# Optimization experiments

Measured on AMD Instinct MI355X. Metric: run time of the kernel, lower is better.

The kernel has to match this reference:

```python
import jax, jax.numpy as jnp
import numpy as np
from jax import lax

B, C_KEY, H, W = 2, 512, 48, 48
HW = H * W
TOPK = 4


def _conv(x, w, b, pad):
    # x: NCHW, w: OIHW (torch Conv2d layout)
    y = lax.conv_general_dilated(x, w, (1, 1), [(pad, pad), (pad, pad)],
                                 dimension_numbers=('NCHW', 'OIHW', 'NCHW'))
    return y + b[None, :, None, None]


def _deconv(x, w, b, stride, pad):
    # torch ConvTranspose2d weight layout (in_c, out_c, kh, kw).
    # Equivalent dilated conv: flip kernel spatially, swap in/out,
    # lhs_dilation=stride, padding=k-1-p each side.
    k = w.shape[2]
    kern = jnp.transpose(jnp.flip(w, (2, 3)), (1, 0, 2, 3))  # OIHW
    y = lax.conv_general_dilated(x, kern, (1, 1),
                                 [(k - 1 - pad, k - 1 - pad)] * 2,
                                 lhs_dilation=(stride, stride),
                                 dimension_numbers=('NCHW', 'OIHW', 'NCHW'))
    return y + b[None, :, None, None]


def setup_inputs() -> dict:
    key = jax.random.key(0)
    ks = jax.random.split(key, 32)

    def nrm(i, shape, scale=1.0):
        return jax.random.normal(ks[i], shape, jnp.float32) * scale

    def unit_key(i):
        k_ = jax.random.normal(ks[i], (B, C_KEY, H, W), jnp.float32)
        return k_ / jnp.linalg.norm(k_, axis=1, keepdims=True)

    inp = {
        'feats_s16': nrm(0, (B, 1024, H, W)),
        'feats_s8': nrm(1, (B, 512, 2 * H, 2 * W)),
        'feats_s4': nrm(2, (B, 256, 4 * H, 4 * W)),
        'key': unit_key(3),
        'init_key': unit_key(4),
        'prev_key': unit_key(5),
        'init_seg_16': jax.random.uniform(ks[6], (B, 2, H, W), jnp.float32),
        'prev_seg_16': jax.random.uniform(ks[7], (B, 2, H, W), jnp.float32),
        'mask_feats': nrm(8, (B, 256, H, W), 0.1),
        # Decoder parameters (torch layouts)
        'w_conv1': nrm(9, (256, 1024, 1, 1), 0.03), 'b_conv1': jnp.zeros((256,), jnp.float32),
        'w_blend1': nrm(10, (256, 516, 3, 3), 0.02), 'b_blend1': jnp.zeros((256,), jnp.float32),
        'w_deconv1': nrm(11, (256, 2, 4, 4), 0.02), 'b_deconv1': jnp.zeros((2,), jnp.float32),
        'w_conv2': nrm(12, (256, 512, 1, 1), 0.04), 'b_conv2': jnp.zeros((256,), jnp.float32),
        'w_blend2': nrm(13, (256, 258, 3, 3), 0.02), 'b_blend2': jnp.zeros((256,), jnp.float32),
        'w_deconv2': nrm(14, (256, 2, 4, 4), 0.02), 'b_deconv2': jnp.zeros((2,), jnp.float32),
        'w_conv3': nrm(15, (256, 256, 1, 1), 0.06), 'b_conv3': jnp.zeros((256,), jnp.float32),
        'w_blend3': nrm(16, (256, 258, 3, 3), 0.02), 'b_blend3': jnp.zeros((256,), jnp.float32),
        'w_deconv3': nrm(17, (256, 2, 6, 6), 0.02), 'b_deconv3': jnp.zeros((2,), jnp.float32),
    }
    return inp


def _forward(feats_s16, feats_s8, feats_s4, key, init_key, prev_key,
             init_seg_16, prev_seg_16, mask_feats,
             w_conv1, b_conv1, w_blend1, b_blend1, w_deconv1, b_deconv1,
             w_conv2, b_conv2, w_blend2, b_blend2, w_deconv2, b_deconv2,
             w_conv3, b_conv3, w_blend3, b_blend3, w_deconv3, b_deconv3):
    relu = jax.nn.relu
    Bn, _, Hh, Ww = key.shape
    HWn = Hh * Ww

    kf = key.reshape(Bn, -1, HWn)
    # cosine similarities mapped to [0,1]; p = ref pixel, q = query pixel
    global_sim = (jnp.einsum('bcp,bcq->bpq', init_key.reshape(Bn, -1, HWn), kf) + 1.0) * 0.5
    local_sim = (jnp.einsum('bcp,bcq->bpq', prev_key.reshape(Bn, -1, HWn), kf) + 1.0) * 0.5

    def global_score(seg_ch):  # seg_ch: (B,H,W)
        s = global_sim * seg_ch.reshape(Bn, HWn, 1)
        return jnp.max(s, axis=1)  # (B,HW)

    def local_score(seg_ch):
        s = local_sim * seg_ch.reshape(Bn, HWn, 1)  # (B,HW,HW)
        cut = lax.top_k(s, TOPK)[0][..., -1:]       # kth-largest along key dim
        mn = jnp.min(s, axis=2, keepdims=True)
        s = jnp.where(s < cut, mn, s)               # threshold masking
        return jnp.max(s, axis=1)                   # (B,HW)

    matching_score = jnp.stack([
        global_score(init_seg_16[:, 0]),
        global_score(init_seg_16[:, 1]),
        local_score(prev_seg_16[:, 0]),
        local_score(prev_seg_16[:, 1]),
    ], axis=1).reshape(Bn, 4, Hh, Ww)

    # Decoder
    x = jnp.concatenate([relu(_conv(feats_s16, w_conv1, b_conv1, 0)),
                         matching_score, mask_feats], axis=1)
    s8 = _deconv(relu(_conv(x, w_blend1, b_blend1, 1)), w_deconv1, b_deconv1, 2, 1)
    x = jnp.concatenate([relu(_conv(feats_s8, w_conv2, b_conv2, 0)), s8], axis=1)
    s4 = _deconv(relu(_conv(x, w_blend2, b_blend2, 1)), w_deconv2, b_deconv2, 2, 1)
    x = jnp.concatenate([relu(_conv(feats_s4, w_conv3, b_conv3, 0)), s4], axis=1)
    final_score = _deconv(relu(_conv(x, w_blend3, b_blend3, 1)), w_deconv3, b_deconv3, 4, 1)
    return final_score


def reference(feats_s16, feats_s8, feats_s4, key, init_key, prev_key,
              init_seg_16, prev_seg_16, mask_feats,
              w_conv1, b_conv1, w_blend1, b_blend1, w_deconv1, b_deconv1,
              w_conv2, b_conv2, w_blend2, b_blend2, w_deconv2, b_deconv2,
              w_conv3, b_conv3, w_blend3, b_blend3, w_deconv3, b_deconv3):
    return _forward(feats_s16, feats_s8, feats_s4, key, init_key, prev_key,
                    init_seg_16, prev_seg_16, mask_feats,
                    w_conv1, b_conv1, w_blend1, b_blend1, w_deconv1, b_deconv1,
                    w_conv2, b_conv2, w_blend2, b_blend2, w_deconv2, b_deconv2,
                    w_conv3, b_conv3, w_blend3, b_blend3, w_deconv3, b_deconv3)
```

## Files before the change

### kernel.cpp

```cpp
#include <hip/hip_runtime.h>
#include <cstdio>

typedef unsigned short u16;
typedef __attribute__((ext_vector_type(4))) float f32x4;
typedef __attribute__((ext_vector_type(8))) short s16x8;
typedef __attribute__((ext_vector_type(4))) unsigned short u16x4;

#define DEV static __device__ __forceinline__

DEV float bf2f(u16 u) { union { unsigned int i; float f; } v; v.i = ((unsigned int)u) << 16; return v.f; }
DEV u16 f2bf(float f) {
  unsigned int x = __float_as_uint(f);
  unsigned int r = (x + 0x7fffu + ((x >> 16) & 1u)) >> 16;
  return (u16)r;
}

typedef const __attribute__((address_space(1))) unsigned int* gptr_t;
typedef __attribute__((address_space(3))) unsigned int* lptr_t;
DEV void gl16(const u16* g, u16* l) {
  __builtin_amdgcn_global_load_lds((gptr_t)g, (lptr_t)l, 16, 0, 0);
}

__global__ __launch_bounds__(256) void trans_key(const float* __restrict__ X,
    u16* __restrict__ Y)
{
  __shared__ u16 t[64][72];
  const int tid = threadIdx.x;
  const int n0 = blockIdx.x * 64, k0 = blockIdx.y * 64, b = blockIdx.z;
  const float* Xb = X + (size_t)b * 512 * 2304;
  const int nl = tid & 63, kr = tid >> 6;
#pragma unroll
  for (int kk = 0; kk < 16; ++kk) {
    int kl = kr + kk * 4;
    t[kl][nl] = f2bf(Xb[(size_t)(k0 + kl) * 2304 + n0 + nl]);
  }
  __syncthreads();
  const int nr = tid >> 2, kb = (tid & 3) * 16;
  u16* yp = Y + (size_t)b * 2304 * 512 + (size_t)(n0 + nr) * 512 + k0 + kb;
#pragma unroll
  for (int i = 0; i < 4; ++i) {
    u16x4 v;
#pragma unroll
    for (int e = 0; e < 4; ++e) v[e] = t[kb + i * 4 + e][nr];
    *(u16x4*)&yp[i * 4] = v;
  }
}

template<int MB>
__global__ __launch_bounds__(256) void sim_gemm_gl(const u16* __restrict__ AT,
    const u16* __restrict__ BT, float* __restrict__ out)
{
  constexpr int SUB = MB / 16, SPW = SUB / 4;
  __shared__ alignas(16) u16 Al[2][SUB][64][8];
  __shared__ alignas(16) u16 Bl[2][4][64][8];
  const int tid = threadIdx.x;
  const int n0 = blockIdx.x * 64, m0 = blockIdx.y * MB, b = blockIdx.z;
  const int lane = tid & 63, wv = tid >> 6;
  const int fr = lane & 15, kq = lane >> 4;
  const u16* Ab = AT + (size_t)b * 2304 * 512;
  const u16* Bb = BT + (size_t)b * 2304 * 512;
  f32x4 acc[SPW][4];
#pragma unroll
  for (int p = 0; p < SPW; ++p)
#pragma unroll
    for (int j = 0; j < 4; ++j) acc[p][j] = (f32x4){0, 0, 0, 0};
  auto ISSUE = [&](int buf, int s) {
    const int k0 = s * 32 + kq * 8;
    gl16(&Bb[(size_t)(n0 + wv * 16 + fr) * 512 + k0], &Bl[buf][wv][0][0]);
#pragma unroll
    for (int p = 0; p < SPW; ++p)
      gl16(&Ab[(size_t)(m0 + (wv * SPW + p) * 16 + fr) * 512 + k0],
           &Al[buf][wv * SPW + p][0][0]);
  };
  ISSUE(0, 0);
  __syncthreads();
  const int NS = 512 / 32;
  for (int s = 0; s < NS; ++s) {
    const int cur = s & 1;
    if (s + 1 < NS) ISSUE(cur ^ 1, s + 1);
    s16x8 bf[4];
#pragma unroll
    for (int j = 0; j < 4; ++j) bf[j] = *(const s16x8*)&Bl[cur][j][lane][0];
#pragma unroll
    for (int p = 0; p < SPW; ++p) {
      s16x8 af = *(const s16x8*)&Al[cur][wv * SPW + p][lane][0];
#pragma unroll
      for (int j = 0; j < 4; ++j)
        acc[p][j] = __builtin_amdgcn_mfma_f32_16x16x32_bf16(af, bf[j], acc[p][j], 0, 0, 0);
    }
    __syncthreads();
  }
  const int col = lane & 15, rg = (lane >> 4) * 4;
#pragma unroll
  for (int p = 0; p < SPW; ++p)
#pragma unroll
    for (int j = 0; j < 4; ++j)
#pragma unroll
      for (int r = 0; r < 4; ++r) {
        int pr = m0 + (wv * SPW + p) * 16 + rg + r;
        int q = n0 + j * 16 + col;
        out[((size_t)b * 2304 + pr) * 2304 + q] = (acc[p][j][r] + 1.0f) * 0.5f;
      }
}

__global__ __launch_bounds__(256) void rowstats(const float* __restrict__ simL,
    float* __restrict__ cutv, float* __restrict__ mnv)
{
  const int row = blockIdx.x;
  const int tid = threadIdx.x;
  const float* r = simL + (size_t)row * 2304;
  float t0 = -1e30f, t1 = -1e30f, t2 = -1e30f, t3 = -1e30f, mn = 1e30f;
  for (int i = tid; i < 2304; i += 256) {
    float v = r[i];
    mn = fminf(mn, v);
    if (v > t3) {
      if (v > t2) { t3 = t2; if (v > t1) { t2 = t1; if (v > t0) { t1 = t0; t0 = v; } else t1 = v; } else t2 = v; }
      else t3 = v;
    }
  }
  __shared__ float s4[256][4];
  __shared__ float smv[256];
  s4[tid][0] = t0; s4[tid][1] = t1; s4[tid][2] = t2; s4[tid][3] = t3;
  smv[tid] = mn;
  __syncthreads();
  for (int s = 128; s > 0; s >>= 1) {
    if (tid < s) {
      float a0 = s4[tid][0], a1 = s4[tid][1], a2 = s4[tid][2], a3 = s4[tid][3];
      float b0 = s4[tid + s][0], b1 = s4[tid + s][1], b2 = s4[tid + s][2], b3 = s4[tid + s][3];
      float m0 = fmaxf(a0, b3), m1 = fmaxf(a1, b2), m2 = fmaxf(a2, b1), m3 = fmaxf(a3, b0);
      float c0 = fmaxf(m0, m2), c2 = fminf(m0, m2), c1 = fmaxf(m1, m3), c3 = fminf(m1, m3);
      s4[tid][0] = fmaxf(c0, c1); s4[tid][1] = fminf(c0, c1);
      s4[tid][2] = fmaxf(c2, c3); s4[tid][3] = fminf(c2, c3);
      smv[tid] = fminf(smv[tid], smv[tid + s]);
    }
    __syncthreads();
  }
  if (tid == 0) { cutv[row] = s4[0][3]; mnv[row] = smv[0]; }
}

__global__ __launch_bounds__(256) void zero_f(float* __restrict__ p, int n)
{
  int i = blockIdx.x * 256 + threadIdx.x;
  if (i < n) p[i] = 0.0f;
}

__global__ __launch_bounds__(256) void zero_u16v(u16* __restrict__ p, long n4)
{
  long i = (long)blockIdx.x * 256 + threadIdx.x;
  const long stride = (long)gridDim.x * 256;
  const uint2 z = {0u, 0u};
  for (; i < n4; i += stride) ((uint2*)p)[i] = z;
}

__global__ __launch_bounds__(256) void score_global(const float* __restrict__ sim,
    const float* __restrict__ seg, float* __restrict__ msc, int chBase)
{
  const int b = blockIdx.z;
  const int q = blockIdx.x * 256 + threadIdx.x;
  const int p0 = blockIdx.y * 128;
  const float* sp = sim + ((size_t)b * 2304 + p0) * 2304 + q;
  const float* sg = seg + (size_t)b * 2 * 2304;
  float m0 = 0.0f, m1 = 0.0f;
  for (int p = 0; p < 128; ++p) {
    float sv = sp[(size_t)p * 2304];
    float s0 = sg[p0 + p];
    float s1 = sg[2304 + p0 + p];
    m0 = fmaxf(m0, sv * s0);
    m1 = fmaxf(m1, sv * s1);
  }
  atomicMax((int*)&msc[((size_t)b * 4 + chBase) * 2304 + q], __float_as_int(m0));
  atomicMax((int*)&msc[((size_t)b * 4 + chBase + 1) * 2304 + q], __float_as_int(m1));
}

__global__ __launch_bounds__(256) void score_local(const float* __restrict__ sim,
    const float* __restrict__ seg, const float* __restrict__ cutv,
    const float* __restrict__ mnv, float* __restrict__ msc, int chBase)
{
  const int b = blockIdx.z;
  const int q = blockIdx.x * 256 + threadIdx.x;
  const int p0 = blockIdx.y * 128;
  const float* sp = sim + ((size_t)b * 2304 + p0) * 2304 + q;
  const float* sg = seg + (size_t)b * 2 * 2304;
  const float* cu = cutv + (size_t)b * 2304 + p0;
  const float* ml = mnv + (size_t)b * 2304 + p0;
  float m0 = 0.0f, m1 = 0.0f;
  for (int p = 0; p < 128; ++p) {
    float sv = sp[(size_t)p * 2304];
    float cut = cu[p], mnr = ml[p];
    float mv = (sv < cut) ? mnr : sv;
    float s0 = sg[p0 + p];
    float s1 = sg[2304 + p0 + p];
    m0 = fmaxf(m0, mv * s0);
    m1 = fmaxf(m1, mv * s1);
  }
  atomicMax((int*)&msc[((size_t)b * 4 + chBase) * 2304 + q], __float_as_int(m0));
  atomicMax((int*)&msc[((size_t)b * 4 + chBase + 1) * 2304 + q], __float_as_int(m1));
}

__global__ __launch_bounds__(256) void fill_scores(const float* __restrict__ msc,
    u16* __restrict__ x1)
{
  int idx = blockIdx.x * 256 + threadIdx.x;
  if (idx >= 2 * 2304) return;
  int b = idx / 2304, q = idx % 2304;
  int py = q / 48, px = q % 48;
  u16x4 v;
#pragma unroll
  for (int c = 0; c < 4; ++c) v[c] = f2bf(msc[((size_t)b * 4 + c) * 2304 + q]);
  *(u16x4*)&x1[((size_t)b * 2500 + (py + 1) * 50 + px + 1) * 544 + 256] = v;
}

__global__ __launch_bounds__(256) void copy_mask(const float* __restrict__ mask,
    u16* __restrict__ x1)
{
  int idx = blockIdx.x * 256 + threadIdx.x;
  if (idx >= 2 * 256 * 2304) return;
  int b = idx / (256 * 2304);
  int r = idx % (256 * 2304);
  int c = r / 2304, q = r % 2304;
  int py = q / 48, px = q % 48;
  x1[((size_t)b * 2500 + (py + 1) * 50 + px + 1) * 544 + 260 + c] = f2bf(mask[idx]);
}

__global__ __launch_bounds__(256) void repack(const float* __restrict__ w,
    u16* __restrict__ wr, int IC, int ICp)
{
  int idx = blockIdx.x * 256 + threadIdx.x;
  int total = 9 * 256 * ICp;
  if (idx >= total) return;
  int ic = idx % ICp;
  int oc = (idx / ICp) % 256;
  int tap = idx / (ICp * 256);
  wr[idx] = (ic < IC) ? f2bf(w[((size_t)oc * IC + ic) * 9 + tap]) : (u16)0;
}

__global__ __launch_bounds__(256) void repack_w(const float* __restrict__ w,
    u16* __restrict__ o, int n)
{
  int i = blockIdx.x * 256 + threadIdx.x;
  if (i < n) o[i] = f2bf(w[i]);
}

__global__ __launch_bounds__(256) void repack_dec(const float* __restrict__ w,
    u16* __restrict__ wr, int S, int KSZ, int MT)
{
  int idx = blockIdx.x * 256 + threadIdx.x;
  int total = MT * 16 * 1024;
  if (idx >= total) return;
  int m = idx >> 10, k = idx & 1023;
  int oc = m & 1, ph = m >> 1;
  int tap = k >> 8, ic = k & 255;
  int dy = tap >> 1, dx = tap & 1;
  float val = 0.0f;
  if (ph < S * S) {
    int ry = ph / S, rx = ph % S;
    int ky = ry + S * dy, kx = rx + S * dx;
    if (ky < KSZ && kx < KSZ)
      val = w[((size_t)(ic * 2 + oc) * KSZ + ky) * KSZ + kx];
  }
  wr[idx] = f2bf(val);
}

template<int MB>
__global__ __launch_bounds__(256) void conv1x1_gl(const float* __restrict__ X,
    const u16* __restrict__ Wb, const float* __restrict__ bias,
    u16* __restrict__ Y, int K, int WD, int Cp)
{
  const int N = WD * WD;
  const int P = WD + 2, HWp = P * P;
  constexpr int SUB = MB / 16, SPW = SUB / 4;
  __shared__ alignas(16) u16 Al[2][SUB][64][8];
  __shared__ alignas(16) u16 Bl[2][4][64][8];
  const int tid = threadIdx.x;
  const int n0 = blockIdx.x * 64, m0 = blockIdx.y * MB, b = blockIdx.z;
  const int lane = tid & 63, wv = tid >> 6;
  const int fr = lane & 15, kq = lane >> 4;
  const float* Xb = X + (size_t)b * K * N;
  const int bpix = n0 + wv * 16 + fr;
  f32x4 acc[SPW][4];
#pragma unroll
  for (int p = 0; p < SPW; ++p)
#pragma unroll
    for (int j = 0; j < 4; ++j) acc[p][j] = (f32x4){0, 0, 0, 0};
  s16x8 bN;
  auto ISSUEA = [&](int buf, int s) {
    const int k0 = s * 32 + kq * 8;
#pragma unroll
    for (int p = 0; p < SPW; ++p)
      gl16(&Wb[(size_t)(m0 + (wv * SPW + p) * 16 + fr) * K + k0],
           &Al[buf][wv * SPW + p][0][0]);
  };
  auto LDB = [&](int s) {
    const int k0 = s * 32;
#pragma unroll
    for (int i = 0; i < 8; ++i)
      bN[i] = (short)f2bf(Xb[(size_t)(k0 + kq * 8 + i) * N + bpix]);
  };
  ISSUEA(0, 0); LDB(0);
  *(s16x8*)&Bl[0][wv][lane][0] = bN;
  __syncthreads();
  const int NS = K / 32;
  for (int s = 0; s < NS; ++s) {
    const int cur = s & 1;
    const bool more = (s + 1) < NS;
    if (more) { ISSUEA(cur ^ 1, s + 1); LDB(s + 1); }
    s16x8 bf[4];
#pragma unroll
    for (int j = 0; j < 4; ++j) bf[j] = *(const s16x8*)&Bl[cur][j][lane][0];
#pragma unroll
    for (int p = 0; p < SPW; ++p) {
      s16x8 af = *(const s16x8*)&Al[cur][wv * SPW + p][lane][0];
#pragma unroll
      for (int j = 0; j < 4; ++j)
        acc[p][j] = __builtin_amdgcn_mfma_f32_16x16x32_bf16(af, bf[j], acc[p][j], 0, 0, 0);
    }
    if (more) *(s16x8*)&Bl[cur ^ 1][wv][lane][0] = bN;
    __syncthreads();
  }
  const int col = lane & 15, rg = (lane >> 4) * 4;
#pragma unroll
  for (int j = 0; j < 4; ++j) {
    const int nn = n0 + j * 16 + col;
    const int py = nn / WD, px = nn % WD;
    const size_t rowb = ((size_t)b * HWp + (py + 1) * P + px + 1) * Cp;
#pragma unroll
    for (int p = 0; p < SPW; ++p) {
      const int oc0 = m0 + (wv * SPW + p) * 16 + rg;
      u16x4 v;
#pragma unroll
      for (int r = 0; r < 4; ++r)
        v[r] = f2bf(fmaxf(acc[p][j][r] + bias[oc0 + r], 0.0f));
      *(u16x4*)&Y[rowb + oc0] = v;
    }
  }
}

template<int WD, int MB>
__global__ __launch_bounds__(256) void blend3x3_gl(const u16* __restrict__ X,
    const u16* __restrict__ Wr, const float* __restrict__ bias,
    u16* __restrict__ Y, int ICp)
{
  constexpr int P = WD + 2, HWp = P * P, HW = WD * WD;
  constexpr int SUB = MB / 16, SPW = SUB / 4;
  __shared__ alignas(16) u16 Al[2][SUB][64][8];
  __shared__ alignas(16) u16 Bl[2][4][64][8];
  const int tid = threadIdx.x;
  const int lane = tid & 63, wv = tid >> 6;
  const int fr = lane & 15, kq = lane >> 4;
  const int n0 = blockIdx.x * 64, m0 = blockIdx.y * MB, b = blockIdx.z;
  const int KS = ICp / 32, NS = 9 * KS;
  const u16* Xb = X + (size_t)b * HWp * ICp;
  const int bpix = n0 + wv * 16 + fr;
  const int brow = (bpix / WD + 1) * P + (bpix % WD) + 1;
  f32x4 acc[SPW][4];
#pragma unroll
  for (int p = 0; p < SPW; ++p)
#pragma unroll
    for (int j = 0; j < 4; ++j) acc[p][j] = (f32x4){0, 0, 0, 0};
  auto ISSUE = [&](int buf, int s) {
    const int tap = s / KS, k0 = (s - tap * KS) * 32 + kq * 8;
    const int dy = tap / 3 - 1, dx = tap % 3 - 1;
    gl16(&Xb[(size_t)(brow + dy * P + dx) * ICp + k0], &Bl[buf][wv][0][0]);
    const u16* wt = Wr + (size_t)tap * 256 * ICp + k0;
#pragma unroll
    for (int p = 0; p < SPW; ++p)
      gl16(&wt[(size_t)(m0 + (wv * SPW + p) * 16 + fr) * ICp],
           &Al[buf][wv * SPW + p][0][0]);
  };
  ISSUE(0, 0);
  __syncthreads();
  for (int s = 0; s < NS; ++s) {
    const int cur = s & 1;
    if (s + 1 < NS) ISSUE(cur ^ 1, s + 1);
    s16x8 bf[4];
#pragma unroll
    for (int j = 0; j < 4; ++j) bf[j] = *(const s16x8*)&Bl[cur][j][lane][0];
#pragma unroll
    for (int p = 0; p < SPW; ++p) {
      s16x8 af = *(const s16x8*)&Al[cur][wv * SPW + p][lane][0];
#pragma unroll
      for (int j = 0; j < 4; ++j)
        acc[p][j] = __builtin_amdgcn_mfma_f32_16x16x32_bf16(af, bf[j], acc[p][j], 0, 0, 0);
    }
    __syncthreads();
  }
  const int col = lane & 15, rg = (lane >> 4) * 4;
#pragma unroll
  for (int j = 0; j < 4; ++j) {
    const int nn = n0 + j * 16 + col;
    const size_t rowb = ((size_t)b * HW + nn) * 256;
#pragma unroll
    for (int p = 0; p < SPW; ++p) {
      const int oc0 = m0 + (wv * SPW + p) * 16 + rg;
      u16x4 v;
#pragma unroll
      for (int r = 0; r < 4; ++r)
        v[r] = f2bf(fmaxf(acc[p][j][r] + bias[oc0 + r], 0.0f));
      *(u16x4*)&Y[rowb + oc0] = v;
    }
  }
}

template<int S, int WIN, int MT, bool F32OUT>
__global__ __launch_bounds__(256) void deconv_dir(const u16* __restrict__ X,
    const u16* __restrict__ Wr, const float* __restrict__ bias,
    void* __restrict__ Yout, int Cp, int coff)
{
  constexpr int NP1 = WIN + 1;
  constexpr int Np = NP1 * NP1;
  constexpr int WO = S * WIN;
  constexpr int HWin = WIN * WIN;
  constexpr int Pout = WO + 2, HWpo = Pout * Pout;
  const int tid = threadIdx.x;
  const int lane = tid & 63, wv = tid >> 6;
  const int fr = lane & 15, kq = lane >> 4;
  const int n0 = blockIdx.x * 64, b = blockIdx.y;
  const u16* Xb = X + (size_t)b * HWin * 256 + kq * 8;
  const int pixn = n0 + wv * 16 + fr;
  const int t_y = pixn / NP1, t_x = pixn % NP1;
  f32x4 acc[MT];
#pragma unroll
  for (int mt = 0; mt < MT; ++mt) acc[mt] = (f32x4){0, 0, 0, 0};
#pragma unroll
  for (int tap = 0; tap < 4; ++tap) {
    const int dy = tap >> 1, dx = tap & 1;
    const int iy = t_y - dy, ix = t_x - dx;
    const bool vsp = (pixn < Np) && ((unsigned)iy < (unsigned)WIN) && ((unsigned)ix < (unsigned)WIN);
    const u16* bpt = Xb + (size_t)(vsp ? iy * WIN + ix : 0) * 256;
    for (int kk = 0; kk < 256; kk += 32) {
      s16x8 bf = *(const s16x8*)(bpt + kk);
      if (!vsp) {
#pragma unroll
        for (int i = 0; i < 8; ++i) bf[i] = 0;
      }
#pragma unroll
      for (int mt = 0; mt < MT; ++mt) {
        s16x8 af = *(const s16x8*)&Wr[(size_t)(mt * 16 + fr) * 1024 + tap * 256 + kk + kq * 8];
        acc[mt] = __builtin_amdgcn_mfma_f32_16x16x32_bf16(af, bf, acc[mt], 0, 0, 0);
      }
    }
  }
  const int col = lane & 15, rg = (lane >> 4) * 4;
  const int nn = n0 + wv * 16 + col;
  if (nn >= Np) return;
  const int oty = nn / NP1, otx = nn % NP1;
#pragma unroll
  for (int mt = 0; mt < MT; ++mt) {
#pragma unroll
    for (int r = 0; r < 4; ++r) {
      int m = mt * 16 + rg + r;
      int ph = m >> 1, oc = m & 1;
      if (ph >= S * S) continue;
      int ry = ph / S, rx = ph % S;
      int oy = S * oty + ry - 1, ox = S * otx + rx - 1;
      if ((unsigned)oy >= (unsigned)WO || (unsigned)ox >= (unsigned)WO) continue;
      float v = acc[mt][r] + bias[oc];
      if (F32OUT)
        ((float*)Yout)[((size_t)b * 2 + oc) * WO * WO + (size_t)oy * WO + ox] = v;
      else
        ((u16*)Yout)[((size_t)b * HWpo + (oy + 1) * Pout + ox + 1) * Cp + coff + oc] = f2bf(v);
    }
  }
}

extern "C" void kernel_launch(void* const* d_in, const int* in_sizes, int n_in,
                              void* d_out, int out_size, void* d_ws, size_t ws_size,
                              hipStream_t stream)
{
  const float* feats_s16 = (const float*)d_in[0];
  const float* feats_s8  = (const float*)d_in[1];
  const float* feats_s4  = (const float*)d_in[2];
  const float* key       = (const float*)d_in[3];
  const float* init_key  = (const float*)d_in[4];
  const float* prev_key  = (const float*)d_in[5];
  const float* init_seg  = (const float*)d_in[6];
  const float* prev_seg  = (const float*)d_in[7];
  const float* mask_f    = (const float*)d_in[8];
  const float* w_conv1 = (const float*)d_in[9];  const float* b_conv1 = (const float*)d_in[10];
  const float* w_blend1= (const float*)d_in[11]; const float* b_blend1= (const float*)d_in[12];
  const float* w_dec1  = (const float*)d_in[13]; const float* b_dec1  = (const float*)d_in[14];
  const float* w_conv2 = (const float*)d_in[15]; const float* b_conv2 = (const float*)d_in[16];
  const float* w_blend2= (const float*)d_in[17]; const float* b_blend2= (const float*)d_in[18];
  const float* w_dec2  = (const float*)d_in[19]; const float* b_dec2  = (const float*)d_in[20];
  const float* w_conv3 = (const float*)d_in[21]; const float* b_conv3 = (const float*)d_in[22];
  const float* w_blend3= (const float*)d_in[23]; const float* b_blend3= (const float*)d_in[24];
  const float* w_dec3  = (const float*)d_in[25]; const float* b_dec3  = (const float*)d_in[26];

  char* ws = (char*)d_ws;
  size_t o = 0;
  auto take = [&](size_t n) { size_t r = o; o += (n + 255) & ~(size_t)255; return r; };
  float* simG = (float*)(ws + take((size_t)2 * 2304 * 2304 * 4));
  float* simL = (float*)(ws + take((size_t)2 * 2304 * 2304 * 4));
  float* cutv = (float*)(ws + take((size_t)2 * 2304 * 4));
  float* mnv  = (float*)(ws + take((size_t)2 * 2304 * 4));
  float* msc  = (float*)(ws + take((size_t)2 * 4 * 2304 * 4));
  u16* x1  = (u16*)(ws + take((size_t)2 * 2500 * 544 * 2));
  u16* b1o = (u16*)(ws + take((size_t)2 * 2304 * 256 * 2));
  u16* x2  = (u16*)(ws + take((size_t)2 * 9604 * 288 * 2));
  u16* b2o = (u16*)(ws + take((size_t)2 * 9216 * 256 * 2));
  u16* x3  = (u16*)(ws + take((size_t)2 * 37636 * 288 * 2));
  u16* b3o = (u16*)(ws + take((size_t)2 * 36864 * 256 * 2));
  u16* wr1 = (u16*)(ws + take((size_t)9 * 256 * 544 * 2));
  u16* wr2 = (u16*)(ws + take((size_t)9 * 256 * 288 * 2));
  u16* wr3 = (u16*)(ws + take((size_t)9 * 256 * 288 * 2));
  u16* wd1r = (u16*)(ws + take((size_t)16 * 1024 * 2));
  u16* wd2r = (u16*)(ws + take((size_t)16 * 1024 * 2));
  u16* wd3r = (u16*)(ws + take((size_t)32 * 1024 * 2));
  u16* keyT = (u16*)(ws + take((size_t)2 * 2304 * 512 * 2));
  u16* ikT  = (u16*)(ws + take((size_t)2 * 2304 * 512 * 2));
  u16* pkT  = (u16*)(ws + take((size_t)2 * 2304 * 512 * 2));
  u16* wc1b = (u16*)(ws + take((size_t)256 * 1024 * 2));
  u16* wc2b = (u16*)(ws + take((size_t)256 * 512 * 2));
  u16* wc3b = (u16*)(ws + take((size_t)256 * 256 * 2));
  if (o > ws_size) {
    fprintf(stderr, "kernel_launch: ws too small: need %zu, have %zu\n", o, ws_size);
    return;
  }

  zero_u16v<<<dim3(2048), 256, 0, stream>>>(x1, (long)2 * 2500 * 544 / 4);
  zero_u16v<<<dim3(2048), 256, 0, stream>>>(x2, (long)2 * 9604 * 288 / 4);
  zero_u16v<<<dim3(2048), 256, 0, stream>>>(x3, (long)2 * 37636 * 288 / 4);
  repack<<<dim3((9 * 256 * 544 + 255) / 256), 256, 0, stream>>>(w_blend1, wr1, 516, 544);
  repack<<<dim3((9 * 256 * 288 + 255) / 256), 256, 0, stream>>>(w_blend2, wr2, 258, 288);
  repack<<<dim3((9 * 256 * 288 + 255) / 256), 256, 0, stream>>>(w_blend3, wr3, 258, 288);
  repack_dec<<<dim3(64), 256, 0, stream>>>(w_dec1, wd1r, 2, 4, 1);
  repack_dec<<<dim3(64), 256, 0, stream>>>(w_dec2, wd2r, 2, 4, 1);
  repack_dec<<<dim3(128), 256, 0, stream>>>(w_dec3, wd3r, 4, 6, 2);
  repack_w<<<dim3(1024), 256, 0, stream>>>(w_conv1, wc1b, 256 * 1024);
  repack_w<<<dim3(512), 256, 0, stream>>>(w_conv2, wc2b, 256 * 512);
  repack_w<<<dim3(256), 256, 0, stream>>>(w_conv3, wc3b, 256 * 256);
  trans_key<<<dim3(36, 8, 2), 256, 0, stream>>>(key, keyT);
  trans_key<<<dim3(36, 8, 2), 256, 0, stream>>>(init_key, ikT);
  trans_key<<<dim3(36, 8, 2), 256, 0, stream>>>(prev_key, pkT);

  sim_gemm_gl<128><<<dim3(36, 18, 2), 256, 0, stream>>>(ikT, keyT, simG);
  sim_gemm_gl<128><<<dim3(36, 18, 2), 256, 0, stream>>>(pkT, keyT, simL);

  rowstats<<<dim3(2 * 2304), 256, 0, stream>>>(simL, cutv, mnv);
  zero_f<<<dim3(72), 256, 0, stream>>>(msc, 2 * 4 * 2304);
  score_global<<<dim3(9, 18, 2), 256, 0, stream>>>(simG, init_seg, msc, 0);
  score_local<<<dim3(9, 18, 2), 256, 0, stream>>>(simL, prev_seg, cutv, mnv, msc, 2);

  conv1x1_gl<64><<<dim3(36, 4, 2), 256, 0, stream>>>(feats_s16, wc1b, b_conv1, x1, 1024, 48, 544);
  fill_scores<<<dim3(18), 256, 0, stream>>>(msc, x1);
  copy_mask<<<dim3(4608), 256, 0, stream>>>(mask_f, x1);
  blend3x3_gl<48, 64><<<dim3(36, 4, 2), 256, 0, stream>>>(x1, wr1, b_blend1, b1o, 544);
  deconv_dir<2, 48, 1, false><<<dim3((49 * 49 + 63) / 64, 2), 256, 0, stream>>>(
      b1o, wd1r, b_dec1, x2, 288, 256);

  conv1x1_gl<128><<<dim3(144, 2, 2), 256, 0, stream>>>(feats_s8, wc2b, b_conv2, x2, 512, 96, 288);
  blend3x3_gl<96, 128><<<dim3(144, 2, 2), 256, 0, stream>>>(x2, wr2, b_blend2, b2o, 288);
  deconv_dir<2, 96, 1, false><<<dim3((97 * 97 + 63) / 64, 2), 256, 0, stream>>>(
      b2o, wd2r, b_dec2, x3, 288, 256);

  conv1x1_gl<128><<<dim3(576, 2, 2), 256, 0, stream>>>(feats_s4, wc3b, b_conv3, x3, 256, 192, 288);
  blend3x3_gl<192, 128><<<dim3(576, 2, 2), 256, 0, stream>>>(x3, wr3, b_blend3, b3o, 288);
  deconv_dir<4, 192, 2, true><<<dim3((193 * 193 + 63) / 64, 2), 256, 0, stream>>>(
      b3o, wd3r, b_dec3, d_out, 2, 0);
}
```

Measured before the change: 727.7 us.

## Store similarity matrices in bf16, use 128x128 GEMM tiles, swap grid order

The similarity GEMM now writes bf16 instead of fp32 and uses a 128x128 tile with a 2x2 wave layout. Each wave now loads four A and four B fragments per step, so operand reuse per LDS read goes up. Rowstats and the score kernels read the bf16 matrices, which halves the traffic on the large 2304x2304 intermediates. The conv launches also swap grid x/y so that blocks sharing a pixel tile run next to each other, which may help L2 reuse of input tiles. Storing in bf16 lowers precision, so top-k cutoffs and max scores may shift slightly.

Result: no change. 735.4 us (+1.1%).

```diff
diff --git a/kernel.cpp b/kernel.cpp
--- a/kernel.cpp
+++ b/kernel.cpp
@@ -46,31 +46,31 @@
   }
 }
 
-template<int MB>
-__global__ __launch_bounds__(256) void sim_gemm_gl(const u16* __restrict__ AT,
-    const u16* __restrict__ BT, float* __restrict__ out)
-{
-  constexpr int SUB = MB / 16, SPW = SUB / 4;
-  __shared__ alignas(16) u16 Al[2][SUB][64][8];
-  __shared__ alignas(16) u16 Bl[2][4][64][8];
+__global__ __launch_bounds__(256) void sim_gemm_128(const u16* __restrict__ AT,
+    const u16* __restrict__ BT, u16* __restrict__ out)
+{
+  __shared__ alignas(16) u16 Al[2][8][64][8];
+  __shared__ alignas(16) u16 Bl[2][8][64][8];
   const int tid = threadIdx.x;
-  const int n0 = blockIdx.x * 64, m0 = blockIdx.y * MB, b = blockIdx.z;
   const int lane = tid & 63, wv = tid >> 6;
   const int fr = lane & 15, kq = lane >> 4;
+  const int wr = wv >> 1, wc = wv & 1;
+  const int n0 = blockIdx.x * 128, m0 = blockIdx.y * 128, b = blockIdx.z;
   const u16* Ab = AT + (size_t)b * 2304 * 512;
   const u16* Bb = BT + (size_t)b * 2304 * 512;
-  f32x4 acc[SPW][4];
-#pragma unroll
-  for (int p = 0; p < SPW; ++p)
+  const int ar0 = m0 + wv * 16 + fr, ar1 = m0 + (wv + 4) * 16 + fr;
+  const int br0 = n0 + wv * 16 + fr, br1 = n0 + (wv + 4) * 16 + fr;
+  f32x4 acc[4][4];
+#pragma unroll
+  for (int p = 0; p < 4; ++p)
 #pragma unroll
     for (int j = 0; j < 4; ++j) acc[p][j] = (f32x4){0, 0, 0, 0};
   auto ISSUE = [&](int buf, int s) {
     const int k0 = s * 32 + kq * 8;
-    gl16(&Bb[(size_t)(n0 + wv * 16 + fr) * 512 + k0], &Bl[buf][wv][0][0]);
-#pragma unroll
-    for (int p = 0; p < SPW; ++p)
-      gl16(&Ab[(size_t)(m0 + (wv * SPW + p) * 16 + fr) * 512 + k0],
-           &Al[buf][wv * SPW + p][0][0]);
+    gl16(&Ab[(size_t)ar0 * 512 + k0], &Al[buf][wv][0][0]);
+    gl16(&Ab[(size_t)ar1 * 512 + k0], &Al[buf][wv + 4][0][0]);
+    gl16(&Bb[(size_t)br0 * 512 + k0], &Bl[buf][wv][0][0]);
+    gl16(&Bb[(size_t)br1 * 512 + k0], &Bl[buf][wv + 4][0][0]);
   };
   ISSUE(0, 0);
   __syncthreads();
@@ -78,40 +78,40 @@
   for (int s = 0; s < NS; ++s) {
     const int cur = s & 1;
     if (s + 1 < NS) ISSUE(cur ^ 1, s + 1);
-    s16x8 bf[4];
-#pragma unroll
-    for (int j = 0; j < 4; ++j) bf[j] = *(const s16x8*)&Bl[cur][j][lane][0];
-#pragma unroll
-    for (int p = 0; p < SPW; ++p) {
-      s16x8 af = *(const s16x8*)&Al[cur][wv * SPW + p][lane][0];
+    s16x8 bf[4], af[4];
+#pragma unroll
+    for (int j = 0; j < 4; ++j) bf[j] = *(const s16x8*)&Bl[cur][wc * 4 + j][lane][0];
+#pragma unroll
+    for (int p = 0; p < 4; ++p) af[p] = *(const s16x8*)&Al[cur][wr * 4 + p][lane][0];
+#pragma unroll
+    for (int p = 0; p < 4; ++p)
 #pragma unroll
       for (int j = 0; j < 4; ++j)
-        acc[p][j] = __builtin_amdgcn_mfma_f32_16x16x32_bf16(af, bf[j], acc[p][j], 0, 0, 0);
-    }
+        acc[p][j] = __builtin_amdgcn_mfma_f32_16x16x32_bf16(af[p], bf[j], acc[p][j], 0, 0, 0);
     __syncthreads();
   }
   const int col = lane & 15, rg = (lane >> 4) * 4;
 #pragma unroll
-  for (int p = 0; p < SPW; ++p)
+  for (int p = 0; p < 4; ++p)
 #pragma unroll
     for (int j = 0; j < 4; ++j)
 #pragma unroll
       for (int r = 0; r < 4; ++r) {
-        int pr = m0 + (wv * SPW + p) * 16 + rg + r;
-        int q = n0 + j * 16 + col;
-        out[((size_t)b * 2304 + pr) * 2304 + q] = (acc[p][j][r] + 1.0f) * 0.5f;
+        int pr = m0 + (wr * 4 + p) * 16 + rg + r;
+        int q = n0 + (wc * 4 + j) * 16 + col;
+        out[((size_t)b * 2304 + pr) * 2304 + q] = f2bf((acc[p][j][r] + 1.0f) * 0.5f);
       }
 }
 
-__global__ __launch_bounds__(256) void rowstats(const float* __restrict__ simL,
+__global__ __launch_bounds__(256) void rowstats(const u16* __restrict__ simL,
     float* __restrict__ cutv, float* __restrict__ mnv)
 {
   const int row = blockIdx.x;
   const int tid = threadIdx.x;
-  const float* r = simL + (size_t)row * 2304;
+  const u16* r = simL + (size_t)row * 2304;
   float t0 = -1e30f, t1 = -1e30f, t2 = -1e30f, t3 = -1e30f, mn = 1e30f;
   for (int i = tid; i < 2304; i += 256) {
-    float v = r[i];
+    float v = bf2f(r[i]);
     mn = fminf(mn, v);
     if (v > t3) {
       if (v > t2) { t3 = t2; if (v > t1) { t2 = t1; if (v > t0) { t1 = t0; t0 = v; } else t1 = v; } else t2 = v; }
@@ -152,17 +152,17 @@
   for (; i < n4; i += stride) ((uint2*)p)[i] = z;
 }
 
-__global__ __launch_bounds__(256) void score_global(const float* __restrict__ sim,
+__global__ __launch_bounds__(256) void score_global(const u16* __restrict__ sim,
     const float* __restrict__ seg, float* __restrict__ msc, int chBase)
 {
   const int b = blockIdx.z;
   const int q = blockIdx.x * 256 + threadIdx.x;
   const int p0 = blockIdx.y * 128;
-  const float* sp = sim + ((size_t)b * 2304 + p0) * 2304 + q;
+  const u16* sp = sim + ((size_t)b * 2304 + p0) * 2304 + q;
   const float* sg = seg + (size_t)b * 2 * 2304;
   float m0 = 0.0f, m1 = 0.0f;
   for (int p = 0; p < 128; ++p) {
-    float sv = sp[(size_t)p * 2304];
+    float sv = bf2f(sp[(size_t)p * 2304]);
     float s0 = sg[p0 + p];
     float s1 = sg[2304 + p0 + p];
     m0 = fmaxf(m0, sv * s0);
@@ -172,20 +172,20 @@
   atomicMax((int*)&msc[((size_t)b * 4 + chBase + 1) * 2304 + q], __float_as_int(m1));
 }
 
-__global__ __launch_bounds__(256) void score_local(const float* __restrict__ sim,
+__global__ __launch_bounds__(256) void score_local(const u16* __restrict__ sim,
     const float* __restrict__ seg, const float* __restrict__ cutv,
     const float* __restrict__ mnv, float* __restrict__ msc, int chBase)
 {
   const int b = blockIdx.z;
   const int q = blockIdx.x * 256 + threadIdx.x;
   const int p0 = blockIdx.y * 128;
-  const float* sp = sim + ((size_t)b * 2304 + p0) * 2304 + q;
+  const u16* sp = sim + ((size_t)b * 2304 + p0) * 2304 + q;
   const float* sg = seg + (size_t)b * 2 * 2304;
   const float* cu = cutv + (size_t)b * 2304 + p0;
   const float* ml = mnv + (size_t)b * 2304 + p0;
   float m0 = 0.0f, m1 = 0.0f;
   for (int p = 0; p < 128; ++p) {
-    float sv = sp[(size_t)p * 2304];
+    float sv = bf2f(sp[(size_t)p * 2304]);
     float cut = cu[p], mnr = ml[p];
     float mv = (sv < cut) ? mnr : sv;
     float s0 = sg[p0 + p];
@@ -272,7 +272,7 @@
   __shared__ alignas(16) u16 Al[2][SUB][64][8];
   __shared__ alignas(16) u16 Bl[2][4][64][8];
   const int tid = threadIdx.x;
-  const int n0 = blockIdx.x * 64, m0 = blockIdx.y * MB, b = blockIdx.z;
+  const int m0 = blockIdx.x * MB, n0 = blockIdx.y * 64, b = blockIdx.z;
   const int lane = tid & 63, wv = tid >> 6;
   const int fr = lane & 15, kq = lane >> 4;
   const float* Xb = X + (size_t)b * K * N;
@@ -347,7 +347,7 @@
   const int tid = threadIdx.x;
   const int lane = tid & 63, wv = tid >> 6;
   const int fr = lane & 15, kq = lane >> 4;
-  const int n0 = blockIdx.x * 64, m0 = blockIdx.y * MB, b = blockIdx.z;
+  const int m0 = blockIdx.x * MB, n0 = blockIdx.y * 64, b = blockIdx.z;
   const int KS = ICp / 32, NS = 9 * KS;
   const u16* Xb = X + (size_t)b * HWp * ICp;
   const int bpix = n0 + wv * 16 + fr;
@@ -489,8 +489,8 @@
   char* ws = (char*)d_ws;
   size_t o = 0;
   auto take = [&](size_t n) { size_t r = o; o += (n + 255) & ~(size_t)255; return r; };
-  float* simG = (float*)(ws + take((size_t)2 * 2304 * 2304 * 4));
-  float* simL = (float*)(ws + take((size_t)2 * 2304 * 2304 * 4));
+  u16* simG = (u16*)(ws + take((size_t)2 * 2304 * 2304 * 2));
+  u16* simL = (u16*)(ws + take((size_t)2 * 2304 * 2304 * 2));
   float* cutv = (float*)(ws + take((size_t)2 * 2304 * 4));
   float* mnv  = (float*)(ws + take((size_t)2 * 2304 * 4));
   float* msc  = (float*)(ws + take((size_t)2 * 4 * 2304 * 4));
@@ -533,28 +533,28 @@
   trans_key<<<dim3(36, 8, 2), 256, 0, stream>>>(init_key, ikT);
   trans_key<<<dim3(36, 8, 2), 256, 0, stream>>>(prev_key, pkT);
 
-  sim_gemm_gl<128><<<dim3(36, 18, 2), 256, 0, stream>>>(ikT, keyT, simG);
-  sim_gemm_gl<128><<<dim3(36, 18, 2), 256, 0, stream>>>(pkT, keyT, simL);
+  sim_gemm_128<<<dim3(18, 18, 2), 256, 0, stream>>>(ikT, keyT, simG);
+  sim_gemm_128<<<dim3(18, 18, 2), 256, 0, stream>>>(pkT, keyT, simL);
 
   rowstats<<<dim3(2 * 2304), 256, 0, stream>>>(simL, cutv, mnv);
   zero_f<<<dim3(72), 256, 0, stream>>>(msc, 2 * 4 * 2304);
   score_global<<<dim3(9, 18, 2), 256, 0, stream>>>(simG, init_seg, msc, 0);
   score_local<<<dim3(9, 18, 2), 256, 0, stream>>>(simL, prev_seg, cutv, mnv, msc, 2);
 
-  conv1x1_gl<64><<<dim3(36, 4, 2), 256, 0, stream>>>(feats_s16, wc1b, b_conv1, x1, 1024, 48, 544);
+  conv1x1_gl<64><<<dim3(4, 36, 2), 256, 0, stream>>>(feats_s16, wc1b, b_conv1, x1, 1024, 48, 544);
   fill_scores<<<dim3(18), 256, 0, stream>>>(msc, x1);
   copy_mask<<<dim3(4608), 256, 0, stream>>>(mask_f, x1);
-  blend3x3_gl<48, 64><<<dim3(36, 4, 2), 256, 0, stream>>>(x1, wr1, b_blend1, b1o, 544);
+  blend3x3_gl<48, 64><<<dim3(4, 36, 2), 256, 0, stream>>>(x1, wr1, b_blend1, b1o, 544);
   deconv_dir<2, 48, 1, false><<<dim3((49 * 49 + 63) / 64, 2), 256, 0, stream>>>(
       b1o, wd1r, b_dec1, x2, 288, 256);
 
-  conv1x1_gl<128><<<dim3(144, 2, 2), 256, 0, stream>>>(feats_s8, wc2b, b_conv2, x2, 512, 96, 288);
-  blend3x3_gl<96, 128><<<dim3(144, 2, 2), 256, 0, stream>>>(x2, wr2, b_blend2, b2o, 288);
+  conv1x1_gl<128><<<dim3(2, 144, 2), 256, 0, stream>>>(feats_s8, wc2b, b_conv2, x2, 512, 96, 288);
+  blend3x3_gl<96, 128><<<dim3(2, 144, 2), 256, 0, stream>>>(x2, wr2, b_blend2, b2o, 288);
   deconv_dir<2, 96, 1, false><<<dim3((97 * 97 + 63) / 64, 2), 256, 0, stream>>>(
       b2o, wd2r, b_dec2, x3, 288, 256);
 
-  conv1x1_gl<128><<<dim3(576, 2, 2), 256, 0, stream>>>(feats_s4, wc3b, b_conv3, x3, 256, 192, 288);
-  blend3x3_gl<192, 128><<<dim3(576, 2, 2), 256, 0, stream>>>(x3, wr3, b_blend3, b3o, 288);
+  conv1x1_gl<128><<<dim3(2, 576, 2), 256, 0, stream>>>(feats_s4, wc3b, b_conv3, x3, 256, 192, 288);
+  blend3x3_gl<192, 128><<<dim3(2, 576, 2), 256, 0, stream>>>(x3, wr3, b_blend3, b3o, 288);
   deconv_dir<4, 192, 2, true><<<dim3((193 * 193 + 63) / 64, 2), 256, 0, stream>>>(
       b3o, wd3r, b_dec3, d_out, 2, 0);
 }
```
